# Optimization experiments

Hardware: AMD Instinct MI355X
Metric: run time of the kernel (lower is better)

The kernel has to match this reference:

```python
import jax, jax.numpy as jnp
import numpy as np

SHIFT = 1  # shift_direction fixed to +1 (original picks +/-1 randomly at init)

def setup_inputs() -> dict:
    key = jax.random.key(0)
    k1, k2, k3 = jax.random.split(key, 3)
    x  = jax.random.normal(k1, (1024, 1792, 28), dtype=jnp.float32)
    w0 = jax.random.normal(k2, (128, 2), dtype=jnp.float32)
    w1 = jax.random.normal(k3, (64, 3, 128), dtype=jnp.float32)
    return {"x": x, "w0": w0, "w1": w1}

def reference(x, w0, w1):
    # unfold (im2col) with kernel (3,1), padding (1,0) along the 28-dim
    xp = jnp.pad(x, ((0, 0), (0, 0), (1, 1)))                 # (1024,1792,30)
    patches = jnp.stack([xp[:, :, k:k + 28] for k in range(3)], axis=2)  # (1024,1792,3,28)
    t3 = patches.reshape(1024, 64, 28, 3, 28)                 # (l,j,m,k,n)
    # einsum 'ljmnk,jki->lmni' (t3 here is in (l,j,m,k,n) order)
    t4 = jnp.einsum('ljmkn,jki->lmni', t3, w1)                # (1024,28,28,128)
    # outer product with w0, directly in the permuted (k,l,i,m,j) order
    t5 = jnp.einsum('klmi,ij->klimj', t4, w0)                 # (1024,28,128,28,2)
    t6 = t5.reshape(1024, 28, 128, 56)
    t6 = jnp.roll(t6, SHIFT, axis=3)
    t6 = t6.reshape(1024, 28, 128, 28, 2).sum(axis=4)         # (1024,28,128,28)
    t7 = jnp.roll(t6, SHIFT, axis=1)
    y = jnp.transpose(t7, (0, 2, 3, 1))                       # (1024,128,28,28)
    return y
```

## Files before the change

kernel.cpp:

```cpp
#include <hip/hip_runtime.h>

typedef short bf16x8 __attribute__((ext_vector_type(8)));
typedef float f32x4 __attribute__((ext_vector_type(4)));
typedef unsigned short u16x4 __attribute__((ext_vector_type(4)));

__device__ __forceinline__ unsigned short f2b(float f) {
    unsigned int u = __builtin_bit_cast(unsigned int, f);
    u += 0x7fffu + ((u >> 16) & 1u);
    return (unsigned short)(u >> 16);
}
__device__ __forceinline__ float b2f(unsigned short s) {
    unsigned int u = ((unsigned int)s) << 16;
    return __builtin_bit_cast(float, u);
}

__global__ void wt_prepass(const float* __restrict__ w1, unsigned short* __restrict__ wt) {
    int t = blockIdx.x * 256 + threadIdx.x;
    if (t >= 24576) return;
    int j = t & 63;
    int i = (t >> 6) & 127;
    int k = t >> 13;
    wt[t] = f2b(w1[(j * 3 + k) * 128 + i]);
}


__global__ __launch_bounds__(256, 2) void fused_main(
        const float* __restrict__ x, const float* __restrict__ w0,
        const unsigned short* __restrict__ wt, float* __restrict__ y) {
    __shared__ __align__(16) char smem[65536];
    __shared__ float w0s[256];

    const int tid  = threadIdx.x;
    const int lane = tid & 63;
    const int w    = tid >> 6;
    const int rl   = lane & 15;
    const int jb0  = (lane >> 4) << 3;

    const int B   = (int)blockIdx.x;
    const int b   = ((B & 7) << 7) + ((B >> 3) >> 2);
    const int bc  = (B >> 3) & 3;
    const int c0  = 7 * bc;

    w0s[tid] = w0[tid];

    {
        int nh = (bc == 0) ? 2 : ((bc == 3) ? 1 : 0);
        for (int idx = tid; idx < nh * 224; idx += 256) {
            int rr = idx;
            int sl;
            if (bc == 0) {
                if (rr >= 224) { sl = 11; rr -= 224; } else sl = 0;
            } else {
                sl = 9;
            }
            int a   = rr >> 3, ch = rr & 7;
            int row = a * 13 + sl;
            int byte = (row << 7) + ((ch << 4) ^ ((row & 7) << 4));
            *reinterpret_cast<f32x4*>(smem + byte) = f32x4{0.f, 0.f, 0.f, 0.f};
        }
    }

    int q0, q1, q2;
    if      (bc == 0) { q0 = 0; q1 = 1; q2 = 6; }
    else if (bc == 1) { q0 = 1; q1 = 2; q2 = 3; }
    else if (bc == 2) { q0 = 3; q1 = 4; q2 = 5; }
    else              { q0 = 4; q1 = 5; q2 = 6; }

    const float* xb = x + (size_t)b * (1792 * 28);
    for (int bt = 0; bt < 3; ++bt) {
        float4 vbuf[7];
#pragma unroll
        for (int u = 0; u < 7; ++u) {
            int f  = tid + (((bt * 7) + u) << 8);
            int R  = f / 3;
            int q3 = f - R * 3;
            int q  = (q3 == 0) ? q0 : ((q3 == 1) ? q1 : q2);
            vbuf[u] = *reinterpret_cast<const float4*>(xb + R * 28 + (q << 2));
        }
#pragma unroll
        for (int u = 0; u < 7; ++u) {
            int f  = tid + (((bt * 7) + u) << 8);
            int R  = f / 3;
            int q3 = f - R * 3;
            int q  = (q3 == 0) ? q0 : ((q3 == 1) ? q1 : q2);
            int a  = R % 28;
            int j2 = (R / 28) << 1;
            float vv[4] = {vbuf[u].x, vbuf[u].y, vbuf[u].z, vbuf[u].w};
#pragma unroll
            for (int e = 0; e < 4; ++e) {
                int n = (q << 2) + e;
                int sl; bool ok;
                if (bc == 0) {
                    if (n < 8)        { sl = n + 1;  ok = true; }
                    else if (n >= 26) { sl = n - 17; ok = true; }
                    else              { sl = 0;      ok = false; }
                } else {
                    sl = n + 2 - c0;
                    ok = (unsigned)sl < 10u;
                }
                if (ok) {
                    int row  = a * 13 + sl;
                    int byte = (row << 7) + (j2 ^ ((row & 7) << 4));
                    *(unsigned short*)(smem + byte) = f2b(vv[e]);
                }
            }
        }
    }
    __syncthreads();

    const int cl = rl & 7;
    const int rh = rl >> 3;
    int rowoff[3];
#pragma unroll
    for (int k = 0; k < 3; ++k) {
        int sIdx = (bc == 0) ? ((cl == 0) ? (9 + k) : (cl - 1 + k)) : (cl + k);
        rowoff[k] = rh * 13 + sIdx;
    }

    f32x4 acc[14][2];
#pragma unroll
    for (int mt = 0; mt < 14; ++mt) {
        acc[mt][0] = f32x4{0.f, 0.f, 0.f, 0.f};
        acc[mt][1] = f32x4{0.f, 0.f, 0.f, 0.f};
    }

#pragma unroll
    for (int s = 0; s < 6; ++s) {
        const int k  = s >> 1;
        const int jb = ((s & 1) << 5) + jb0;
        const int jx = jb << 1;
        bf16x8 b0 = *reinterpret_cast<const bf16x8*>(wt + (k << 13) + (((w << 5) + rl) << 6) + jb);
        bf16x8 b1 = *reinterpret_cast<const bf16x8*>(wt + (k << 13) + (((w << 5) + 16 + rl) << 6) + jb);
#pragma unroll
        for (int mt = 0; mt < 14; ++mt) {
            int row  = 26 * mt + rowoff[k];
            int byte = (row << 7) + (jx ^ ((row & 7) << 4));
            bf16x8 af = *reinterpret_cast<const bf16x8*>(smem + byte);
            acc[mt][0] = __builtin_amdgcn_mfma_f32_16x16x32_bf16(af, b0, acc[mt][0], 0, 0, 0);
            acc[mt][1] = __builtin_amdgcn_mfma_f32_16x16x32_bf16(af, b1, acc[mt][1], 0, 0, 0);
        }
    }
    __syncthreads();

    {
        const int rq  = (lane >> 4) << 2;
        const int icb = (w << 5) + rl;
#pragma unroll
        for (int mt = 0; mt < 14; ++mt) {
            int rbase = (mt << 4) + rq;
            int a     = rbase >> 3;
            int l     = (a == 27) ? 0 : (a + 1);
            int l2    = l << 1;
            int clb   = rbase & 7;
#pragma unroll
            for (int p = 0; p < 2; ++p) {
                int ic   = icb + (p << 4);
                int base = (ic << 9);
                int ic7  = ic * 7;
#pragma unroll
                for (int q = 0; q < 4; ++q) {
                    int cc   = clb + q;
                    int byte = base + (cc << 6) + (l2 ^ (((ic7 + cc) & 7) << 3));
                    *(unsigned short*)(smem + byte) = f2b(acc[mt][p][q]);
                }
            }
        }
    }
    __syncthreads();

    for (int f = tid; f < 6272; f += 256) {
        int lq    = f % 7;
        int t1    = f / 7;
        int m_loc = t1 % 7;
        int iloc  = t1 / 7;
        float w00 = w0s[2 * iloc], w01 = w0s[2 * iloc + 1];
        int m     = c0 + m_loc;
        int lo    = lq << 3;
        int i7    = iloc * 7;
        int cl1   = m_loc + 1;
        int cl2   = m_loc;
        int by1   = (iloc << 9) + (cl1 << 6) + (lo ^ (((i7 + cl1) & 7) << 3));
        int by2   = (iloc << 9) + (cl2 << 6) + (lo ^ (((i7 + cl2) & 7) << 3));
        u16x4 h1  = *reinterpret_cast<const u16x4*>(smem + by1);
        u16x4 h2  = *reinterpret_cast<const u16x4*>(smem + by2);
        f32x4 o;
        o.x = w00 * b2f(h1.x) + w01 * b2f(h2.x);
        o.y = w00 * b2f(h1.y) + w01 * b2f(h2.y);
        o.z = w00 * b2f(h1.z) + w01 * b2f(h2.z);
        o.w = w00 * b2f(h1.w) + w01 * b2f(h2.w);
        __builtin_nontemporal_store(
            o, reinterpret_cast<f32x4*>(y + ((((size_t)b * 128 + iloc) * 28 + m) * 28) + (lq << 2)));
    }
}

extern "C" void kernel_launch(void* const* d_in, const int* in_sizes, int n_in,
                              void* d_out, int out_size, void* d_ws, size_t ws_size,
                              hipStream_t stream) {
    const float* x  = (const float*)d_in[0];
    const float* w0 = (const float*)d_in[1];
    const float* w1 = (const float*)d_in[2];
    float* y = (float*)d_out;
    unsigned short* wt = (unsigned short*)d_ws;

    hipLaunchKernelGGL(wt_prepass, dim3(96), dim3(256), 0, stream, w1, wt);
    hipLaunchKernelGGL(fused_main, dim3(4096), dim3(256), 0, stream, x, w0, wt, y);
}
```

Baseline: 175.9 us.

## Split output channels across two blocks to shrink LDS and raise occupancy

Each block now computes 64 of the 128 output channels instead of all 128. The grid doubles to 8192 blocks, the accumulator array halves, shared memory drops to about 46KB, and launch bounds ask for 3 blocks per CU. The aim is more resident waves to hide memory latency. The cost is that each x tile is loaded from global memory and converted to bf16 twice, once per channel half, which doubles input traffic and staging work.

```diff
diff --git a/kernel.cpp b/kernel.cpp
--- a/kernel.cpp
+++ b/kernel.cpp
@@ -24,10 +24,10 @@
 }
 
 
-__global__ __launch_bounds__(256, 2) void fused_main(
+__global__ __launch_bounds__(256, 3) void fused_main(
         const float* __restrict__ x, const float* __restrict__ w0,
         const unsigned short* __restrict__ wt, float* __restrict__ y) {
-    __shared__ __align__(16) char smem[65536];
+    __shared__ __align__(16) char smem[46592];
     __shared__ float w0s[256];
 
     const int tid  = threadIdx.x;
@@ -36,10 +36,14 @@
     const int rl   = lane & 15;
     const int jb0  = (lane >> 4) << 3;
 
-    const int B   = (int)blockIdx.x;
-    const int b   = ((B & 7) << 7) + ((B >> 3) >> 2);
-    const int bc  = (B >> 3) & 3;
-    const int c0  = 7 * bc;
+    const int B     = (int)blockIdx.x;
+    const int xcd   = B & 7;
+    const int g     = B >> 3;
+    const int bc    = g & 3;
+    const int ih    = (g >> 2) & 1;
+    const int bslot = g >> 3;
+    const int b     = (xcd << 7) + bslot;
+    const int c0    = 7 * bc;
 
     w0s[tid] = w0[tid];
 
@@ -117,34 +121,31 @@
         rowoff[k] = rh * 13 + sIdx;
     }
 
-    f32x4 acc[14][2];
-#pragma unroll
-    for (int mt = 0; mt < 14; ++mt) {
-        acc[mt][0] = f32x4{0.f, 0.f, 0.f, 0.f};
-        acc[mt][1] = f32x4{0.f, 0.f, 0.f, 0.f};
-    }
+    const int iglob = (ih << 6) + (w << 4) + rl;
+
+    f32x4 acc[14];
+#pragma unroll
+    for (int mt = 0; mt < 14; ++mt) acc[mt] = f32x4{0.f, 0.f, 0.f, 0.f};
 
 #pragma unroll
     for (int s = 0; s < 6; ++s) {
         const int k  = s >> 1;
         const int jb = ((s & 1) << 5) + jb0;
         const int jx = jb << 1;
-        bf16x8 b0 = *reinterpret_cast<const bf16x8*>(wt + (k << 13) + (((w << 5) + rl) << 6) + jb);
-        bf16x8 b1 = *reinterpret_cast<const bf16x8*>(wt + (k << 13) + (((w << 5) + 16 + rl) << 6) + jb);
+        bf16x8 bf = *reinterpret_cast<const bf16x8*>(wt + (k << 13) + (iglob << 6) + jb);
 #pragma unroll
         for (int mt = 0; mt < 14; ++mt) {
             int row  = 26 * mt + rowoff[k];
             int byte = (row << 7) + (jx ^ ((row & 7) << 4));
             bf16x8 af = *reinterpret_cast<const bf16x8*>(smem + byte);
-            acc[mt][0] = __builtin_amdgcn_mfma_f32_16x16x32_bf16(af, b0, acc[mt][0], 0, 0, 0);
-            acc[mt][1] = __builtin_amdgcn_mfma_f32_16x16x32_bf16(af, b1, acc[mt][1], 0, 0, 0);
+            acc[mt] = __builtin_amdgcn_mfma_f32_16x16x32_bf16(af, bf, acc[mt], 0, 0, 0);
         }
     }
     __syncthreads();
 
     {
         const int rq  = (lane >> 4) << 2;
-        const int icb = (w << 5) + rl;
+        const int icb = (w << 4) + rl;
 #pragma unroll
         for (int mt = 0; mt < 14; ++mt) {
             int rbase = (mt << 4) + rq;
@@ -152,28 +153,25 @@
             int l     = (a == 27) ? 0 : (a + 1);
             int l2    = l << 1;
             int clb   = rbase & 7;
-#pragma unroll
-            for (int p = 0; p < 2; ++p) {
-                int ic   = icb + (p << 4);
-                int base = (ic << 9);
-                int ic7  = ic * 7;
-#pragma unroll
-                for (int q = 0; q < 4; ++q) {
-                    int cc   = clb + q;
-                    int byte = base + (cc << 6) + (l2 ^ (((ic7 + cc) & 7) << 3));
-                    *(unsigned short*)(smem + byte) = f2b(acc[mt][p][q]);
-                }
+            int base  = (icb << 9);
+            int ic7   = icb * 7;
+#pragma unroll
+            for (int q = 0; q < 4; ++q) {
+                int cc   = clb + q;
+                int byte = base + (cc << 6) + (l2 ^ (((ic7 + cc) & 7) << 3));
+                *(unsigned short*)(smem + byte) = f2b(acc[mt][q]);
             }
         }
     }
     __syncthreads();
 
-    for (int f = tid; f < 6272; f += 256) {
+    for (int f = tid; f < 3136; f += 256) {
         int lq    = f % 7;
         int t1    = f / 7;
         int m_loc = t1 % 7;
         int iloc  = t1 / 7;
-        float w00 = w0s[2 * iloc], w01 = w0s[2 * iloc + 1];
+        int ig    = (ih << 6) + iloc;
+        float w00 = w0s[2 * ig], w01 = w0s[2 * ig + 1];
         int m     = c0 + m_loc;
         int lo    = lq << 3;
         int i7    = iloc * 7;
@@ -189,7 +187,7 @@
         o.z = w00 * b2f(h1.z) + w01 * b2f(h2.z);
         o.w = w00 * b2f(h1.w) + w01 * b2f(h2.w);
         __builtin_nontemporal_store(
-            o, reinterpret_cast<f32x4*>(y + ((((size_t)b * 128 + iloc) * 28 + m) * 28) + (lq << 2)));
+            o, reinterpret_cast<f32x4*>(y + ((((size_t)b * 128 + ig) * 28 + m) * 28) + (lq << 2)));
     }
 }
 
@@ -203,5 +201,5 @@
     unsigned short* wt = (unsigned short*)d_ws;
 
     hipLaunchKernelGGL(wt_prepass, dim3(96), dim3(256), 0, stream, w1, wt);
-    hipLaunchKernelGGL(fused_main, dim3(4096), dim3(256), 0, stream, x, w0, wt, y);
-}
+    hipLaunchKernelGGL(fused_main, dim3(8192), dim3(256), 0, stream, x, w0, wt, y);
+}
```

After: 198.9 us. 1.13x slower.

## Double block size to 512 threads, splitting MFMA rows across two wave groups

Applied to the files above, without the earlier changes.

Raises the block from 256 to 512 threads. The 8 waves split the 14 M-tiles into two halves of 7 while keeping the 4-way split over output channels, so each wave holds half as many accumulators. The input load and the output store loops are restructured and fully unrolled over the larger thread count. The aim is more memory-level parallelism and waves per CU at lower per-thread register use. The block still needs 64KB of LDS, so the number of resident blocks per CU is unchanged, and the weight fragments are now loaded by twice as many waves.

```diff
diff --git a/kernel.cpp b/kernel.cpp
--- a/kernel.cpp
+++ b/kernel.cpp
@@ -24,7 +24,7 @@
 }
 
 
-__global__ __launch_bounds__(256, 2) void fused_main(
+__global__ __launch_bounds__(512, 4) void fused_main(
         const float* __restrict__ x, const float* __restrict__ w0,
         const unsigned short* __restrict__ wt, float* __restrict__ y) {
     __shared__ __align__(16) char smem[65536];
@@ -41,11 +41,11 @@
     const int bc  = (B >> 3) & 3;
     const int c0  = 7 * bc;
 
-    w0s[tid] = w0[tid];
+    if (tid < 256) w0s[tid] = w0[tid];
 
     {
         int nh = (bc == 0) ? 2 : ((bc == 3) ? 1 : 0);
-        for (int idx = tid; idx < nh * 224; idx += 256) {
+        for (int idx = tid; idx < nh * 224; idx += 512) {
             int rr = idx;
             int sl;
             if (bc == 0) {
@@ -67,49 +67,55 @@
     else              { q0 = 4; q1 = 5; q2 = 6; }
 
     const float* xb = x + (size_t)b * (1792 * 28);
-    for (int bt = 0; bt < 3; ++bt) {
-        float4 vbuf[7];
-#pragma unroll
-        for (int u = 0; u < 7; ++u) {
-            int f  = tid + (((bt * 7) + u) << 8);
-            int R  = f / 3;
-            int q3 = f - R * 3;
-            int q  = (q3 == 0) ? q0 : ((q3 == 1) ? q1 : q2);
-            vbuf[u] = *reinterpret_cast<const float4*>(xb + R * 28 + (q << 2));
-        }
-#pragma unroll
-        for (int u = 0; u < 7; ++u) {
-            int f  = tid + (((bt * 7) + u) << 8);
-            int R  = f / 3;
-            int q3 = f - R * 3;
-            int q  = (q3 == 0) ? q0 : ((q3 == 1) ? q1 : q2);
-            int a  = R % 28;
-            int j2 = (R / 28) << 1;
-            float vv[4] = {vbuf[u].x, vbuf[u].y, vbuf[u].z, vbuf[u].w};
-#pragma unroll
-            for (int e = 0; e < 4; ++e) {
-                int n = (q << 2) + e;
-                int sl; bool ok;
-                if (bc == 0) {
-                    if (n < 8)        { sl = n + 1;  ok = true; }
-                    else if (n >= 26) { sl = n - 17; ok = true; }
-                    else              { sl = 0;      ok = false; }
-                } else {
-                    sl = n + 2 - c0;
-                    ok = (unsigned)sl < 10u;
+    {
+        float4 vbuf[11];
+#pragma unroll
+        for (int u = 0; u < 11; ++u) {
+            int f = tid + (u << 9);
+            if (f < 5376) {
+                int R  = f / 3;
+                int q3 = f - R * 3;
+                int q  = (q3 == 0) ? q0 : ((q3 == 1) ? q1 : q2);
+                vbuf[u] = *reinterpret_cast<const float4*>(xb + R * 28 + (q << 2));
+            }
+        }
+#pragma unroll
+        for (int u = 0; u < 11; ++u) {
+            int f = tid + (u << 9);
+            if (f < 5376) {
+                int R  = f / 3;
+                int q3 = f - R * 3;
+                int q  = (q3 == 0) ? q0 : ((q3 == 1) ? q1 : q2);
+                int a  = R % 28;
+                int j2 = (R / 28) << 1;
+                float vv[4] = {vbuf[u].x, vbuf[u].y, vbuf[u].z, vbuf[u].w};
+#pragma unroll
+                for (int e = 0; e < 4; ++e) {
+                    int n = (q << 2) + e;
+                    int sl; bool ok;
+                    if (bc == 0) {
+                        if (n < 8)        { sl = n + 1;  ok = true; }
+                        else if (n >= 26) { sl = n - 17; ok = true; }
+                        else              { sl = 0;      ok = false; }
+                    } else {
+                        sl = n + 2 - c0;
+                        ok = (unsigned)sl < 10u;
+                    }
+                    if (ok) {
+                        int row  = a * 13 + sl;
+                        int byte = (row << 7) + (j2 ^ ((row & 7) << 4));
+                        *(unsigned short*)(smem + byte) = f2b(vv[e]);
+                    }
                 }
-                if (ok) {
-                    int row  = a * 13 + sl;
-                    int byte = (row << 7) + (j2 ^ ((row & 7) << 4));
-                    *(unsigned short*)(smem + byte) = f2b(vv[e]);
-                }
             }
         }
     }
     __syncthreads();
 
-    const int cl = rl & 7;
-    const int rh = rl >> 3;
+    const int cl  = rl & 7;
+    const int rh  = rl >> 3;
+    const int mt0 = (w >> 2) * 7;
+    const int wn  = w & 3;
     int rowoff[3];
 #pragma unroll
     for (int k = 0; k < 3; ++k) {
@@ -117,9 +123,9 @@
         rowoff[k] = rh * 13 + sIdx;
     }
 
-    f32x4 acc[14][2];
-#pragma unroll
-    for (int mt = 0; mt < 14; ++mt) {
+    f32x4 acc[7][2];
+#pragma unroll
+    for (int mt = 0; mt < 7; ++mt) {
         acc[mt][0] = f32x4{0.f, 0.f, 0.f, 0.f};
         acc[mt][1] = f32x4{0.f, 0.f, 0.f, 0.f};
     }
@@ -129,11 +135,11 @@
         const int k  = s >> 1;
         const int jb = ((s & 1) << 5) + jb0;
         const int jx = jb << 1;
-        bf16x8 b0 = *reinterpret_cast<const bf16x8*>(wt + (k << 13) + (((w << 5) + rl) << 6) + jb);
-        bf16x8 b1 = *reinterpret_cast<const bf16x8*>(wt + (k << 13) + (((w << 5) + 16 + rl) << 6) + jb);
-#pragma unroll
-        for (int mt = 0; mt < 14; ++mt) {
-            int row  = 26 * mt + rowoff[k];
+        bf16x8 b0 = *reinterpret_cast<const bf16x8*>(wt + (k << 13) + (((wn << 5) + rl) << 6) + jb);
+        bf16x8 b1 = *reinterpret_cast<const bf16x8*>(wt + (k << 13) + (((wn << 5) + 16 + rl) << 6) + jb);
+#pragma unroll
+        for (int mt = 0; mt < 7; ++mt) {
+            int row  = 26 * (mt0 + mt) + rowoff[k];
             int byte = (row << 7) + (jx ^ ((row & 7) << 4));
             bf16x8 af = *reinterpret_cast<const bf16x8*>(smem + byte);
             acc[mt][0] = __builtin_amdgcn_mfma_f32_16x16x32_bf16(af, b0, acc[mt][0], 0, 0, 0);
@@ -144,10 +150,10 @@
 
     {
         const int rq  = (lane >> 4) << 2;
-        const int icb = (w << 5) + rl;
-#pragma unroll
-        for (int mt = 0; mt < 14; ++mt) {
-            int rbase = (mt << 4) + rq;
+        const int icb = (wn << 5) + rl;
+#pragma unroll
+        for (int mt = 0; mt < 7; ++mt) {
+            int rbase = ((mt0 + mt) << 4) + rq;
             int a     = rbase >> 3;
             int l     = (a == 27) ? 0 : (a + 1);
             int l2    = l << 1;
@@ -168,28 +174,32 @@
     }
     __syncthreads();
 
-    for (int f = tid; f < 6272; f += 256) {
-        int lq    = f % 7;
-        int t1    = f / 7;
-        int m_loc = t1 % 7;
-        int iloc  = t1 / 7;
-        float w00 = w0s[2 * iloc], w01 = w0s[2 * iloc + 1];
-        int m     = c0 + m_loc;
-        int lo    = lq << 3;
-        int i7    = iloc * 7;
-        int cl1   = m_loc + 1;
-        int cl2   = m_loc;
-        int by1   = (iloc << 9) + (cl1 << 6) + (lo ^ (((i7 + cl1) & 7) << 3));
-        int by2   = (iloc << 9) + (cl2 << 6) + (lo ^ (((i7 + cl2) & 7) << 3));
-        u16x4 h1  = *reinterpret_cast<const u16x4*>(smem + by1);
-        u16x4 h2  = *reinterpret_cast<const u16x4*>(smem + by2);
-        f32x4 o;
-        o.x = w00 * b2f(h1.x) + w01 * b2f(h2.x);
-        o.y = w00 * b2f(h1.y) + w01 * b2f(h2.y);
-        o.z = w00 * b2f(h1.z) + w01 * b2f(h2.z);
-        o.w = w00 * b2f(h1.w) + w01 * b2f(h2.w);
-        __builtin_nontemporal_store(
-            o, reinterpret_cast<f32x4*>(y + ((((size_t)b * 128 + iloc) * 28 + m) * 28) + (lq << 2)));
+#pragma unroll
+    for (int u = 0; u < 13; ++u) {
+        int f = tid + (u << 9);
+        if (f < 6272) {
+            int lq    = f % 7;
+            int t1    = f / 7;
+            int m_loc = t1 % 7;
+            int iloc  = t1 / 7;
+            float w00 = w0s[2 * iloc], w01 = w0s[2 * iloc + 1];
+            int m     = c0 + m_loc;
+            int lo    = lq << 3;
+            int i7    = iloc * 7;
+            int cl1   = m_loc + 1;
+            int cl2   = m_loc;
+            int by1   = (iloc << 9) + (cl1 << 6) + (lo ^ (((i7 + cl1) & 7) << 3));
+            int by2   = (iloc << 9) + (cl2 << 6) + (lo ^ (((i7 + cl2) & 7) << 3));
+            u16x4 h1  = *reinterpret_cast<const u16x4*>(smem + by1);
+            u16x4 h2  = *reinterpret_cast<const u16x4*>(smem + by2);
+            f32x4 o;
+            o.x = w00 * b2f(h1.x) + w01 * b2f(h2.x);
+            o.y = w00 * b2f(h1.y) + w01 * b2f(h2.y);
+            o.z = w00 * b2f(h1.z) + w01 * b2f(h2.z);
+            o.w = w00 * b2f(h1.w) + w01 * b2f(h2.w);
+            __builtin_nontemporal_store(
+                o, reinterpret_cast<f32x4*>(y + ((((size_t)b * 128 + iloc) * 28 + m) * 28) + (lq << 2)));
+        }
     }
 }
 
@@ -203,5 +213,5 @@
     unsigned short* wt = (unsigned short*)d_ws;
 
     hipLaunchKernelGGL(wt_prepass, dim3(96), dim3(256), 0, stream, w1, wt);
-    hipLaunchKernelGGL(fused_main, dim3(4096), dim3(256), 0, stream, x, w0, wt, y);
-}
+    hipLaunchKernelGGL(fused_main, dim3(4096), dim3(512), 0, stream, x, w0, wt, y);
+}
```

After: 172.3 us. -2.0%, faster.
